# Kernel tuning notes

Hardware: AMD Instinct MI355X
Metric: run time of the kernel (lower is better)

## Reference

```python
import jax, jax.numpy as jnp
import numpy as np

H, D = 8, 16
NA, NB, E, F = 50000, 50000, 200000, 128
SQRT_D = float(np.sqrt(D))


def _proj(x, W, b):
    # Linear then split heads: [N, F] -> [N, H, D]
    return (x @ W + b).reshape(x.shape[0], H, D)


def _seg_softmax(alpha, idx, n):
    # softmax over edges sharing the same destination node (per head)
    amax = jax.ops.segment_max(alpha, idx, num_segments=n)
    amax = jnp.where(jnp.isfinite(amax), amax, 0.0)
    ex = jnp.exp(alpha - amax[idx])
    den = jax.ops.segment_sum(ex, idx, num_segments=n)
    return ex / (den[idx] + 1e-16)


def _hgt_conv(xa, xb, eis, Wk, bk, Wq, bq, Wv, bv, Wa, ba, skip, arel, mrel, prel):
    # node types: 0='a', 1='b'; edge types: 0 a->b, 1 b->a, 2 a->a
    xs = (xa, xb)
    k = [_proj(xs[t], Wk[t], bk[t]) for t in range(2)]
    q = [_proj(xs[t], Wq[t], bq[t]) for t in range(2)]
    v = [_proj(xs[t], Wv[t], bv[t]) for t in range(2)]
    nn_ = (xa.shape[0], xb.shape[0])
    agg = [jnp.zeros((nn_[t], H, D), xa.dtype) for t in range(2)]
    spec = ((0, 1, eis[0]), (1, 0, eis[1]), (0, 0, eis[2]))
    for e, (s, d, ei) in enumerate(spec):
        src, dst = ei[0], ei[1]
        k_rel = jnp.einsum('nhd,hde->nhe', k[s], arel[e])  # [Ns,H,D]
        v_rel = jnp.einsum('nhd,hde->nhe', v[s], mrel[e])
        alpha = jnp.sum(q[d][dst] * k_rel[src], axis=-1) * prel[e] / SQRT_D  # [E,H]
        w = _seg_softmax(alpha, dst, nn_[d])
        agg[d] = agg[d] + jax.ops.segment_sum(v_rel[src] * w[..., None], dst, num_segments=nn_[d])
    outs = []
    for t in range(2):
        o = jax.nn.gelu(agg[t].reshape(-1, H * D), approximate=False) @ Wa[t] + ba[t]
        sgate = jax.nn.sigmoid(skip[t])  # learned skip-gate, dims match so always applied
        outs.append(sgate * o + (1.0 - sgate) * xs[t])
    return outs[0], outs[1]


def _forward(xa, xb, eis, Wk, bk, Wq, bq, Wv, bv, Wa, ba, skip, arel, mrel, prel):
    for l in range(2):
        xa, xb = _hgt_conv(xa, xb, eis, Wk[l], bk[l], Wq[l], bq[l], Wv[l], bv[l],
                           Wa[l], ba[l], skip[l], arel[l], mrel[l], prel[l])
        if l < 1:
            xa, xb = jax.nn.relu(xa), jax.nn.relu(xb)  # dropout: identity in eval mode
    return xa, xb


def setup_inputs() -> dict:
    key = jax.random.key(0)
    ks = jax.random.split(key, 12)
    s = 0.05
    return {
        'xa': jax.random.normal(ks[0], (NA, F), jnp.float32),
        'xb': jax.random.normal(ks[1], (NB, F), jnp.float32),
        'ei_ab': jax.random.randint(ks[2], (2, E), 0, NA, dtype=jnp.int32),
        'ei_ba': jax.random.randint(ks[3], (2, E), 0, NB, dtype=jnp.int32),
        'ei_aa': jax.random.randint(ks[4], (2, E), 0, NA, dtype=jnp.int32),
        'Wk': jax.random.normal(ks[5], (2, 2, F, F), jnp.float32) * s,
        'bk': jnp.zeros((2, 2, F), jnp.float32),
        'Wq': jax.random.normal(ks[6], (2, 2, F, F), jnp.float32) * s,
        'bq': jnp.zeros((2, 2, F), jnp.float32),
        'Wv': jax.random.normal(ks[7], (2, 2, F, F), jnp.float32) * s,
        'bv': jnp.zeros((2, 2, F), jnp.float32),
        'Wa': jax.random.normal(ks[8], (2, 2, F, F), jnp.float32) * s,
        'ba': jnp.zeros((2, 2, F), jnp.float32),
        'skip': jnp.zeros((2, 2), jnp.float32),
        'arel': jax.random.normal(ks[9], (2, 3, H, D, D), jnp.float32) * (1.0 / SQRT_D),
        'mrel': jax.random.normal(ks[10], (2, 3, H, D, D), jnp.float32) * (1.0 / SQRT_D),
        'prel': jnp.ones((2, 3, H), jnp.float32),
    }


def reference(xa, xb, ei_ab, ei_ba, ei_aa, Wk, bk, Wq, bq, Wv, bv, Wa, ba, skip, arel, mrel, prel):
    return _forward(xa, xb, (ei_ab, ei_ba, ei_aa), Wk, bk, Wq, bq, Wv, bv, Wa, ba, skip, arel, mrel, prel)
```

## Files before the change

### kernel.cpp

```cpp
#include <hip/hip_runtime.h>
#include <hip/hip_bf16.h>
#include <math.h>

#define F 128
#define NH 8
#define HD 16

static inline int cdiv(int a, int b) { return (a + b - 1) / b; }

typedef __attribute__((ext_vector_type(8))) short bf16x8;
typedef __attribute__((ext_vector_type(4))) float f32x4;

__device__ __forceinline__ float geluf(float x) {
    return 0.5f * x * (1.f + erff(x * 0.70710678118654752440f));
}

__device__ __forceinline__ short f2bf(float f) {
    __hip_bfloat16 h = __float2bfloat16(f);
    return *reinterpret_cast<short*>(&h);
}

__device__ __forceinline__ float bflo(unsigned int u) { return __uint_as_float(u << 16); }
__device__ __forceinline__ float bfhi(unsigned int u) { return __uint_as_float(u & 0xffff0000u); }
__device__ __forceinline__ float bf2f(short s) {
    return __uint_as_float(((unsigned int)(unsigned short)s) << 16);
}
__device__ __forceinline__ unsigned int packbf(float a, float b) {
    return (unsigned int)(unsigned short)f2bf(a) | ((unsigned int)(unsigned short)f2bf(b) << 16);
}

__device__ __forceinline__ void glds16(const void* g, void* l) {
    __builtin_amdgcn_global_load_lds(
        (const __attribute__((address_space(1))) unsigned int*)g,
        (__attribute__((address_space(3))) unsigned int*)l, 16, 0, 0);
}

__device__ __forceinline__ void slot_info(int slot, int& kind, int& wsel, int& e, int& t) {
    switch (slot) {
        case 0: kind = 0; wsel = 0; t = 0; e = 0; break;
        case 1: kind = 1; wsel = 1; t = 0; e = 0; break;
        case 2: kind = 1; wsel = 2; t = 0; e = 0; break;
        case 3: kind = 1; wsel = 1; t = 0; e = 2; break;
        case 4: kind = 1; wsel = 2; t = 0; e = 2; break;
        case 5: kind = 0; wsel = 0; t = 1; e = 0; break;
        case 6: kind = 1; wsel = 1; t = 1; e = 1; break;
        case 7: kind = 1; wsel = 2; t = 1; e = 1; break;
        case 8: kind = 0; wsel = 3; t = 0; e = 0; break;
        default: kind = 0; wsel = 3; t = 1; e = 0; break;
    }
}

__global__ void prep_all(const float* __restrict__ Wk, const float* __restrict__ bk,
                         const float* __restrict__ Wq, const float* __restrict__ bq,
                         const float* __restrict__ Wv, const float* __restrict__ bv,
                         const float* __restrict__ Wa, const float* __restrict__ ba,
                         const float* __restrict__ arel, const float* __restrict__ mrel,
                         const float* __restrict__ xa, const float* __restrict__ xb,
                         const int* __restrict__ ei0, const int* __restrict__ ei1,
                         const int* __restrict__ ei2,
                         short* __restrict__ Wslots, float* __restrict__ bslots,
                         short* __restrict__ xab, short* __restrict__ xbb,
                         int* __restrict__ cnt,
                         int NA_, int NB_, int E0, int E1, int E2,
                         int PWB, int CONVB) {
    const int WTOT = 10 * 16384;
    const int bid = blockIdx.x;
    const int tid = threadIdx.x;
    if (bid < 2 * PWB) {
        const int layer = bid / PWB;
        short* Wl = Wslots + (size_t)layer * WTOT;
        float* bl = bslots + (size_t)layer * 10 * 128;
        int idx = (bid % PWB) * 256 + tid;
        if (idx < WTOT) {
            int slot = idx >> 14, rem = idx & 16383;
            int n = rem >> 7, k = rem & 127;
            int kind, wsel, e, t;
            slot_info(slot, kind, wsel, e, t);
            float out;
            if (kind == 0) {
                const float* Wb = (wsel == 0 ? Wq : Wa) + (size_t)(layer * 2 + t) * 16384;
                out = Wb[k * 128 + n];
            } else {
                int h = n >> 4, j = n & 15;
                const float* Wb = (wsel == 1 ? Wk : Wv) + (size_t)(layer * 2 + t) * 16384;
                const float* R = (wsel == 1 ? arel : mrel) + (size_t)((layer * 3 + e) * NH + h) * 256;
                float s = 0.f;
                #pragma unroll
                for (int d = 0; d < HD; ++d) s += Wb[k * 128 + h * 16 + d] * R[d * 16 + j];
                out = s;
            }
            int chunk = k >> 3, kin = k & 7;
            int cph = (chunk + (n & 15)) & 15;
            Wl[(size_t)slot * 16384 + n * 128 + cph * 8 + kin] = f2bf(out);
        } else {
            int r = idx - WTOT;
            if (r < 10 * 128) {
                int slot = r >> 7, n = r & 127;
                int kind, wsel, e, t;
                slot_info(slot, kind, wsel, e, t);
                float out;
                if (kind == 0) {
                    const float* bb = (wsel == 0 ? bq : ba) + (size_t)(layer * 2 + t) * 128;
                    out = bb[n];
                } else {
                    int h = n >> 4, j = n & 15;
                    const float* bb = (wsel == 1 ? bk : bv) + (size_t)(layer * 2 + t) * 128;
                    const float* R = (wsel == 1 ? arel : mrel) + (size_t)((layer * 3 + e) * NH + h) * 256;
                    float s = 0.f;
                    #pragma unroll
                    for (int d = 0; d < HD; ++d) s += bb[h * 16 + d] * R[d * 16 + j];
                    out = s;
                }
                bl[slot * 128 + n] = out;
            }
        }
    } else if (bid < 2 * PWB + CONVB) {
        int gi = (bid - 2 * PWB) * 256 + tid;
        int total8 = (NA_ + NB_) * 16;
        if (gi < total8) {
            size_t e = (size_t)gi * 8;
            const float* src; short* dst; size_t off;
            if (e < (size_t)NA_ * 128) { src = xa; dst = xab; off = e; }
            else { src = xb; dst = xbb; off = e - (size_t)NA_ * 128; }
            float4 v0 = *(const float4*)&src[off];
            float4 v1 = *(const float4*)&src[off + 4];
            bf16x8 s;
            s[0] = f2bf(v0.x); s[1] = f2bf(v0.y); s[2] = f2bf(v0.z); s[3] = f2bf(v0.w);
            s[4] = f2bf(v1.x); s[5] = f2bf(v1.y); s[6] = f2bf(v1.z); s[7] = f2bf(v1.w);
            *(bf16x8*)&dst[off] = s;
        }
    } else {
        int i = (bid - 2 * PWB - CONVB) * 256 + tid;
        if (i >= E0 + E1 + E2) return;
        const int* ei; int li, Ee, base;
        if (i < E0)           { li = i;           ei = ei0; Ee = E0; base = 0; }
        else if (i < E0 + E1) { li = i - E0;      ei = ei1; Ee = E1; base = NB_; }
        else                  { li = i - E0 - E1; ei = ei2; Ee = E2; base = NB_ + NA_; }
        atomicAdd(&cnt[base + ei[Ee + li]], 1);
    }
}

__device__ __forceinline__ short* qkv_slot_ptr(int side, int s,
    short* qA, short* kA0, short* vA0, short* kA2, short* vA2,
    short* qB, short* kB1, short* vB1) {
    if (side) {
        if (s == 0) return qB;
        if (s == 1) return kB1;
        return vB1;
    }
    if (s == 0) return qA;
    if (s == 1) return kA0;
    if (s == 2) return vA0;
    if (s == 3) return kA2;
    return vA2;
}

__device__ __forceinline__ void stage_W(const short* __restrict__ Wt, short* Ws,
                                        int wave, int lane) {
    #pragma unroll
    for (int it = 0; it < 8; ++it) {
        int off = (it * 4 + wave) * 1024;
        glds16((const char*)Wt + off + lane * 16, (char*)Ws + off);
    }
}

__global__ __launch_bounds__(256) void gemm_qkv_all(
    const short* __restrict__ Aa, const short* __restrict__ Ab,
    const short* __restrict__ Wl, const float* __restrict__ bl,
    short* __restrict__ qA, short* __restrict__ kA0, short* __restrict__ vA0,
    short* __restrict__ kA2, short* __restrict__ vA2,
    short* __restrict__ qB, short* __restrict__ kB1, short* __restrict__ vB1,
    int NA_, int NB_, int nbA, int nbGemm,
    const int* __restrict__ cnt, int* __restrict__ offc, int* __restrict__ bsum, int NT) {
    __shared__ __align__(16) float Wsf[64 * 132];
    __shared__ __align__(16) short As[64 * 136];
    __shared__ int slds[256];
    short* Ws = (short*)Wsf;
    const int tid = threadIdx.x;
    const int bid = blockIdx.x;

    if (bid >= nbGemm) {
        int blk = bid - nbGemm;
        int i = blk * 256 + tid;
        int v = (i < NT) ? cnt[i] : 0;
        slds[tid] = v;
        __syncthreads();
        #pragma unroll
        for (int s = 1; s < 256; s <<= 1) {
            int t = (tid >= s) ? slds[tid - s] : 0;
            __syncthreads();
            slds[tid] += t;
            __syncthreads();
        }
        if (i < NT) offc[i] = slds[tid] - v;
        if (tid == 255) bsum[blk] = slds[255];
        return;
    }

    const int side = bid >= nbA;
    const short* A = side ? Ab : Aa;
    const int N = side ? NB_ : NA_;
    const int row0 = (side ? bid - nbA : bid) * 64;
    const short* Wbase = Wl + (side ? (size_t)5 * 16384 : 0);
    const float* bbase = bl + (side ? 5 * 128 : 0);
    const int S = side ? 3 : 5;

    const int wave = tid >> 6;
    const int lane = tid & 63;
    const int m16 = lane & 15;
    const int kg = lane >> 4;
    const int arow = wave * 16 + m16;

    #pragma unroll
    for (int it = 0; it < 4; ++it) {
        int chunk = tid + it * 256;
        int r = chunk >> 4, c8 = (chunk & 15) * 8;
        int gr = row0 + r;
        bf16x8 s = {};
        if (gr < N) s = *(const bf16x8*)&A[(size_t)gr * F + c8];
        *(bf16x8*)&As[r * 136 + c8] = s;
    }
    __syncthreads();

    bf16x8 af[4];
    #pragma unroll
    for (int kq = 0; kq < 4; ++kq)
        af[kq] = *(const bf16x8*)&As[arow * 136 + kq * 32 + kg * 8];

    for (int s = 0; s < S; ++s) {
        if (s) __syncthreads();
        stage_W(Wbase + (size_t)s * 16384, Ws, wave, lane);
        __syncthreads();

        f32x4 acc[8] = {};
        #pragma unroll
        for (int kq = 0; kq < 4; ++kq) {
            #pragma unroll
            for (int nt = 0; nt < 8; ++nt) {
                int cph = (kq * 4 + kg + m16) & 15;
                bf16x8 b = *(const bf16x8*)&Ws[(nt * 16 + m16) * 128 + cph * 8];
                acc[nt] = __builtin_amdgcn_mfma_f32_16x16x32_bf16(af[kq], b, acc[nt], 0, 0, 0);
            }
        }
        __syncthreads();

        #pragma unroll
        for (int nt = 0; nt < 8; ++nt)
            #pragma unroll
            for (int r = 0; r < 4; ++r)
                Wsf[(wave * 16 + kg * 4 + r) * 132 + nt * 16 + m16] = acc[nt][r];
        __syncthreads();

        short* optr = qkv_slot_ptr(side, s, qA, kA0, vA0, kA2, vA2, qB, kB1, vB1);
        const float* bias = bbase + s * 128;
        #pragma unroll
        for (int it = 0; it < 4; ++it) {
            int chunk = tid + it * 256;
            int r = chunk >> 4, c8 = (chunk & 15) * 8;
            int gr = row0 + r;
            if (gr >= N) continue;
            float4 b0 = *(const float4*)&bias[c8];
            float4 b1 = *(const float4*)&bias[c8 + 4];
            float4 va = *(float4*)&Wsf[r * 132 + c8];
            float4 vb = *(float4*)&Wsf[r * 132 + c8 + 4];
            bf16x8 o;
            o[0] = f2bf(va.x + b0.x); o[1] = f2bf(va.y + b0.y);
            o[2] = f2bf(va.z + b0.z); o[3] = f2bf(va.w + b0.w);
            o[4] = f2bf(vb.x + b1.x); o[5] = f2bf(vb.y + b1.y);
            o[6] = f2bf(vb.z + b1.z); o[7] = f2bf(vb.w + b1.w);
            *(bf16x8*)&optr[(size_t)gr * F + c8] = o;
        }
    }
}

__global__ __launch_bounds__(256) void fused_out_qkv(
    const short* __restrict__ aggA, const short* __restrict__ aggB,
    const short* __restrict__ Wl0, const float* __restrict__ bl0,
    const short* __restrict__ xabA, const short* __restrict__ xabB,
    const float* __restrict__ skipp,
    const short* __restrict__ Wl1, const float* __restrict__ bl1,
    short* __restrict__ x1A, short* __restrict__ x1B,
    short* __restrict__ qA, short* __restrict__ kA0, short* __restrict__ vA0,
    short* __restrict__ kA2, short* __restrict__ vA2,
    short* __restrict__ qB, short* __restrict__ kB1, short* __restrict__ vB1,
    int NA_, int NB_, int nbA) {
    __shared__ __align__(16) float Wsf[64 * 132];
    __shared__ __align__(16) short As[64 * 136];
    short* Ws = (short*)Wsf;
    const int tid = threadIdx.x;
    const int bid = blockIdx.x;
    const int side = bid >= nbA;
    const short* A = side ? aggB : aggA;
    const int N = side ? NB_ : NA_;
    const int row0 = (side ? bid - nbA : bid) * 64;
    const short* Wt0 = Wl0 + (size_t)(side ? 9 : 8) * 16384;
    const float* bias0 = bl0 + (side ? 9 : 8) * 128;

    const int wave = tid >> 6;
    const int lane = tid & 63;
    const int m16 = lane & 15;
    const int kg = lane >> 4;
    const int arow = wave * 16 + m16;

    stage_W(Wt0, Ws, wave, lane);
    #pragma unroll
    for (int it = 0; it < 4; ++it) {
        int chunk = tid + it * 256;
        int r = chunk >> 4, c8 = (chunk & 15) * 8;
        int gr = row0 + r;
        bf16x8 s = {};
        if (gr < N) {
            s = *(const bf16x8*)&A[(size_t)gr * F + c8];
            #pragma unroll
            for (int u = 0; u < 8; ++u) s[u] = f2bf(geluf(bf2f(s[u])));
        }
        *(bf16x8*)&As[r * 136 + c8] = s;
    }
    __syncthreads();

    {
        f32x4 acc[8] = {};
        #pragma unroll
        for (int kq = 0; kq < 4; ++kq) {
            bf16x8 a = *(const bf16x8*)&As[arow * 136 + kq * 32 + kg * 8];
            #pragma unroll
            for (int nt = 0; nt < 8; ++nt) {
                int cph = (kq * 4 + kg + m16) & 15;
                bf16x8 b = *(const bf16x8*)&Ws[(nt * 16 + m16) * 128 + cph * 8];
                acc[nt] = __builtin_amdgcn_mfma_f32_16x16x32_bf16(a, b, acc[nt], 0, 0, 0);
            }
        }
        __syncthreads();
        #pragma unroll
        for (int nt = 0; nt < 8; ++nt)
            #pragma unroll
            for (int r = 0; r < 4; ++r)
                Wsf[(wave * 16 + kg * 4 + r) * 132 + nt * 16 + m16] = acc[nt][r];
        __syncthreads();
    }

    {
        float sg = 1.f / (1.f + expf(-skipp[side]));
        short* x1 = side ? x1B : x1A;
        const short* xf = side ? xabB : xabA;
        #pragma unroll
        for (int it = 0; it < 4; ++it) {
            int chunk = tid + it * 256;
            int r = chunk >> 4, c8 = (chunk & 15) * 8;
            int gr = row0 + r;
            if (gr >= N) continue;
            float4 b0 = *(const float4*)&bias0[c8];
            float4 b1 = *(const float4*)&bias0[c8 + 4];
            float4 va = *(float4*)&Wsf[r * 132 + c8];
            float4 vb = *(float4*)&Wsf[r * 132 + c8 + 4];
            bf16x8 xrv = *(const bf16x8*)&xf[(size_t)gr * F + c8];
            float v[8] = {va.x + b0.x, va.y + b0.y, va.z + b0.z, va.w + b0.w,
                          vb.x + b1.x, vb.y + b1.y, vb.z + b1.z, vb.w + b1.w};
            bf16x8 o;
            #pragma unroll
            for (int u = 0; u < 8; ++u)
                o[u] = f2bf(fmaxf(sg * v[u] + (1.f - sg) * bf2f(xrv[u]), 0.f));
            *(bf16x8*)&x1[(size_t)gr * F + c8] = o;
            *(bf16x8*)&As[r * 136 + c8] = o;
        }
    }
    __syncthreads();

    bf16x8 af[4];
    #pragma unroll
    for (int kq = 0; kq < 4; ++kq)
        af[kq] = *(const bf16x8*)&As[arow * 136 + kq * 32 + kg * 8];

    const short* Wbase = Wl1 + (side ? (size_t)5 * 16384 : 0);
    const float* bbase = bl1 + (side ? 5 * 128 : 0);
    const int S = side ? 3 : 5;

    for (int s = 0; s < S; ++s) {
        __syncthreads();
        stage_W(Wbase + (size_t)s * 16384, Ws, wave, lane);
        __syncthreads();

        f32x4 acc[8] = {};
        #pragma unroll
        for (int kq = 0; kq < 4; ++kq) {
            #pragma unroll
            for (int nt = 0; nt < 8; ++nt) {
                int cph = (kq * 4 + kg + m16) & 15;
                bf16x8 b = *(const bf16x8*)&Ws[(nt * 16 + m16) * 128 + cph * 8];
                acc[nt] = __builtin_amdgcn_mfma_f32_16x16x32_bf16(af[kq], b, acc[nt], 0, 0, 0);
            }
        }
        __syncthreads();

        #pragma unroll
        for (int nt = 0; nt < 8; ++nt)
            #pragma unroll
            for (int r = 0; r < 4; ++r)
                Wsf[(wave * 16 + kg * 4 + r) * 132 + nt * 16 + m16] = acc[nt][r];
        __syncthreads();

        short* optr = qkv_slot_ptr(side, s, qA, kA0, vA0, kA2, vA2, qB, kB1, vB1);
        const float* bias = bbase + s * 128;
        #pragma unroll
        for (int it = 0; it < 4; ++it) {
            int chunk = tid + it * 256;
            int r = chunk >> 4, c8 = (chunk & 15) * 8;
            int gr = row0 + r;
            if (gr >= N) continue;
            float4 b0 = *(const float4*)&bias[c8];
            float4 b1 = *(const float4*)&bias[c8 + 4];
            float4 va = *(float4*)&Wsf[r * 132 + c8];
            float4 vb = *(float4*)&Wsf[r * 132 + c8 + 4];
            bf16x8 o;
            o[0] = f2bf(va.x + b0.x); o[1] = f2bf(va.y + b0.y);
            o[2] = f2bf(va.z + b0.z); o[3] = f2bf(va.w + b0.w);
            o[4] = f2bf(vb.x + b1.x); o[5] = f2bf(vb.y + b1.y);
            o[6] = f2bf(vb.z + b1.z); o[7] = f2bf(vb.w + b1.w);
            *(bf16x8*)&optr[(size_t)gr * F + c8] = o;
        }
    }
}

__global__ __launch_bounds__(256) void gemm_out_final(
    const short* __restrict__ aggA, const short* __restrict__ aggB,
    const short* __restrict__ Wl, const float* __restrict__ bl,
    const short* __restrict__ xbA, const short* __restrict__ xbB,
    const float* __restrict__ skipp,
    float* __restrict__ CfA, float* __restrict__ CfB,
    int NA_, int NB_, int nbA) {
    __shared__ __align__(16) float Wsf[64 * 132];
    __shared__ __align__(16) short As[64 * 136];
    short* Ws = (short*)Wsf;
    const int tid = threadIdx.x;
    const int bid = blockIdx.x;
    const int side = bid >= nbA;
    const short* A = side ? aggB : aggA;
    const int N = side ? NB_ : NA_;
    const int row0 = (side ? bid - nbA : bid) * 64;
    const short* Wt = Wl + (size_t)(side ? 9 : 8) * 16384;
    const float* bias = bl + (side ? 9 : 8) * 128;

    const int wave = tid >> 6;
    const int lane = tid & 63;
    const int m16 = lane & 15;
    const int kg = lane >> 4;
    const int arow = wave * 16 + m16;

    stage_W(Wt, Ws, wave, lane);
    #pragma unroll
    for (int it = 0; it < 4; ++it) {
        int chunk = tid + it * 256;
        int r = chunk >> 4, c8 = (chunk & 15) * 8;
        int gr = row0 + r;
        bf16x8 s = {};
        if (gr < N) {
            s = *(const bf16x8*)&A[(size_t)gr * F + c8];
            #pragma unroll
            for (int u = 0; u < 8; ++u) s[u] = f2bf(geluf(bf2f(s[u])));
        }
        *(bf16x8*)&As[r * 136 + c8] = s;
    }
    __syncthreads();

    f32x4 acc[8] = {};
    #pragma unroll
    for (int kq = 0; kq < 4; ++kq) {
        bf16x8 a = *(const bf16x8*)&As[arow * 136 + kq * 32 + kg * 8];
        #pragma unroll
        for (int nt = 0; nt < 8; ++nt) {
            int cph = (kq * 4 + kg + m16) & 15;
            bf16x8 b = *(const bf16x8*)&Ws[(nt * 16 + m16) * 128 + cph * 8];
            acc[nt] = __builtin_amdgcn_mfma_f32_16x16x32_bf16(a, b, acc[nt], 0, 0, 0);
        }
    }
    __syncthreads();

    #pragma unroll
    for (int nt = 0; nt < 8; ++nt)
        #pragma unroll
        for (int r = 0; r < 4; ++r)
            Wsf[(wave * 16 + kg * 4 + r) * 132 + nt * 16 + m16] = acc[nt][r];
    __syncthreads();

    float sg = 1.f / (1.f + expf(-skipp[side]));
    #pragma unroll
    for (int it = 0; it < 4; ++it) {
        int chunk = tid + it * 256;
        int r = chunk >> 4, c8 = (chunk & 15) * 8;
        int gr = row0 + r;
        if (gr >= N) continue;
        float4 b0 = *(const float4*)&bias[c8];
        float4 b1 = *(const float4*)&bias[c8 + 4];
        float4 va = *(float4*)&Wsf[r * 132 + c8];
        float4 vb = *(float4*)&Wsf[r * 132 + c8 + 4];
        float v[8] = {va.x + b0.x, va.y + b0.y, va.z + b0.z, va.w + b0.w,
                      vb.x + b1.x, vb.y + b1.y, vb.z + b1.z, vb.w + b1.w};
        const short* xb = side ? xbB : xbA;
        bf16x8 xrv = *(const bf16x8*)&xb[(size_t)gr * F + c8];
        float* Cf = side ? CfB : CfA;
        float o[8];
        #pragma unroll
        for (int u = 0; u < 8; ++u)
            o[u] = sg * v[u] + (1.f - sg) * bf2f(xrv[u]);
        *(float4*)&Cf[(size_t)gr * F + c8]     = make_float4(o[0], o[1], o[2], o[3]);
        *(float4*)&Cf[(size_t)gr * F + c8 + 4] = make_float4(o[4], o[5], o[6], o[7]);
    }
}


__global__ __launch_bounds__(1024) void scan2(int* __restrict__ bsum, int nb,
                                              int* __restrict__ off_n) {
    __shared__ int lds[1024];
    int tid = threadIdx.x;
    int v = (tid < nb) ? bsum[tid] : 0;
    lds[tid] = v;
    __syncthreads();
    #pragma unroll
    for (int s = 1; s < 1024; s <<= 1) {
        int t = (tid >= s) ? lds[tid - s] : 0;
        __syncthreads();
        lds[tid] += t;
        __syncthreads();
    }
    if (tid < nb) bsum[tid] = lds[tid] - v;
    if (tid == 1023) *off_n = lds[1023];
}

__global__ void scan3(int* __restrict__ off, int* __restrict__ woff,
                      const int* __restrict__ bsum, int n) {
    int i = blockIdx.x * 256 + threadIdx.x;
    if (i < n) {
        int v = off[i] + bsum[blockIdx.x];
        off[i] = v;
        woff[i] = v;
    }
}

__global__ void scatter_all(const int* __restrict__ ei0, const int* __restrict__ ei1,
                            const int* __restrict__ ei2, int E0, int E1, int E2,
                            int NB_, int NA_, int* __restrict__ woff,
                            int* __restrict__ csr_src) {
    int i = blockIdx.x * 256 + threadIdx.x;
    if (i >= E0 + E1 + E2) return;
    const int* ei; int li, Ee, base;
    if (i < E0)           { li = i;           ei = ei0; Ee = E0; base = 0; }
    else if (i < E0 + E1) { li = i - E0;      ei = ei1; Ee = E1; base = NB_; }
    else                  { li = i - E0 - E1; ei = ei2; Ee = E2; base = NB_ + NA_; }
    int p = atomicAdd(&woff[base + ei[Ee + li]], 1);
    csr_src[p] = ei[li] * 16;
}

__device__ __forceinline__ void seg_set4(
    const uint4* __restrict__ kArr, const uint4* __restrict__ vArr,
    int c0, int e1, const int* __restrict__ csr, int s, int p,
    const float* __restrict__ qf, float pr,
    float* __restrict__ accv, float& den) {
    for (; c0 < e1; c0 += 4) {
        int rem = e1 - c0;
        bool act = s < rem;
        int sj = csr[c0 + (act ? s : 0)];
        uint4 kw = kArr[sj + p];
        uint4 vw = vArr[sj + p];
        float d = bflo(kw.x) * qf[0];
        d = fmaf(bfhi(kw.x), qf[1], d);
        d = fmaf(bflo(kw.y), qf[2], d);
        d = fmaf(bfhi(kw.y), qf[3], d);
        d = fmaf(bflo(kw.z), qf[4], d);
        d = fmaf(bfhi(kw.z), qf[5], d);
        d = fmaf(bflo(kw.w), qf[6], d);
        d = fmaf(bfhi(kw.w), qf[7], d);
        d += __shfl_xor(d, 1);
        float ex = __expf(fminf(d * pr, 80.f));
        ex = act ? ex : 0.f;
        den += ex;
        accv[0] = fmaf(ex, bflo(vw.x), accv[0]);
        accv[1] = fmaf(ex, bfhi(vw.x), accv[1]);
        accv[2] = fmaf(ex, bflo(vw.y), accv[2]);
        accv[3] = fmaf(ex, bfhi(vw.y), accv[3]);
        accv[4] = fmaf(ex, bflo(vw.z), accv[4]);
        accv[5] = fmaf(ex, bfhi(vw.z), accv[5]);
        accv[6] = fmaf(ex, bflo(vw.w), accv[6]);
        accv[7] = fmaf(ex, bfhi(vw.w), accv[7]);
    }
}

__device__ __forceinline__ void seg_fold(float* __restrict__ accv, float& den,
                                         float* __restrict__ r) {
    #pragma unroll
    for (int j = 0; j < 8; ++j) {
        accv[j] += __shfl_xor(accv[j], 16);
        accv[j] += __shfl_xor(accv[j], 32);
    }
    den += __shfl_xor(den, 16);
    den += __shfl_xor(den, 32);
    float inv = 1.f / (den + 1e-16f);
    #pragma unroll
    for (int j = 0; j < 8; ++j) r[j] = fmaf(accv[j], inv, r[j]);
}

__global__ __launch_bounds__(256) void seg_attn_all(
    const short* __restrict__ qA, const short* __restrict__ kA0,
    const short* __restrict__ vA0, const short* __restrict__ kA2,
    const short* __restrict__ vA2, const short* __restrict__ qB,
    const short* __restrict__ kB1, const short* __restrict__ vB1,
    const int* __restrict__ off0, const int* __restrict__ off1,
    const int* __restrict__ off2, const int* __restrict__ csrS,
    const float* __restrict__ prelL,
    short* __restrict__ aggA, short* __restrict__ aggB,
    int NA_, int NB_, int nba) {
    const int wv = threadIdx.x >> 6;
    const int l = threadIdx.x & 63;
    const int s = l >> 4;
    const int p = l & 15;
    const int h = p >> 1;
    const int isA = (int)blockIdx.x < nba;
    int dst = (isA ? blockIdx.x : blockIdx.x - nba) * 4 + wv;
    if (dst >= (isA ? NA_ : NB_)) return;

    uint4 qw = ((const uint4*)(isA ? qA : qB))[(size_t)dst * 16 + p];
    float qf[8] = {bflo(qw.x), bfhi(qw.x), bflo(qw.y), bfhi(qw.y),
                   bflo(qw.z), bfhi(qw.z), bflo(qw.w), bfhi(qw.w)};

    float r[8] = {};
    float accv[8] = {};
    float den = 0.f;
    if (isA) {
        seg_set4((const uint4*)kB1, (const uint4*)vB1, off1[dst], off1[dst + 1],
                 csrS, s, p, qf, prelL[1 * NH + h] * 0.25f, accv, den);
        seg_fold(accv, den, r);
        #pragma unroll
        for (int j = 0; j < 8; ++j) accv[j] = 0.f;
        den = 0.f;
        seg_set4((const uint4*)kA2, (const uint4*)vA2, off2[dst], off2[dst + 1],
                 csrS, s, p, qf, prelL[2 * NH + h] * 0.25f, accv, den);
        seg_fold(accv, den, r);
    } else {
        seg_set4((const uint4*)kA0, (const uint4*)vA0, off0[dst], off0[dst + 1],
                 csrS, s, p, qf, prelL[0 * NH + h] * 0.25f, accv, den);
        seg_fold(accv, den, r);
    }
    if (s == 0) {
        uint4 o;
        o.x = packbf(r[0], r[1]);
        o.y = packbf(r[2], r[3]);
        o.z = packbf(r[4], r[5]);
        o.w = packbf(r[6], r[7]);
        ((uint4*)(isA ? aggA : aggB))[(size_t)dst * 16 + p] = o;
    }
}

extern "C" void kernel_launch(void* const* d_in, const int* in_sizes, int n_in,
                              void* d_out, int out_size, void* d_ws, size_t ws_size,
                              hipStream_t stream) {
    const float* xa   = (const float*)d_in[0];
    const float* xb   = (const float*)d_in[1];
    const int* ei_ab  = (const int*)d_in[2];
    const int* ei_ba  = (const int*)d_in[3];
    const int* ei_aa  = (const int*)d_in[4];
    const float* Wk   = (const float*)d_in[5];
    const float* bk   = (const float*)d_in[6];
    const float* Wq   = (const float*)d_in[7];
    const float* bq   = (const float*)d_in[8];
    const float* Wv   = (const float*)d_in[9];
    const float* bv   = (const float*)d_in[10];
    const float* Wa   = (const float*)d_in[11];
    const float* ba   = (const float*)d_in[12];
    const float* skip = (const float*)d_in[13];
    const float* arel = (const float*)d_in[14];
    const float* mrel = (const float*)d_in[15];
    const float* prel = (const float*)d_in[16];

    const int NA = in_sizes[0] / F;
    const int NB = in_sizes[1] / F;
    const int E0 = in_sizes[2] / 2, E1 = in_sizes[3] / 2, E2 = in_sizes[4] / 2;
    const int ET = E0 + E1 + E2;
    const int NT = NB + NA + NA;

    float* ws = (float*)d_ws;
    size_t o = 0;
    float* bslots = ws + o; o += 2 * 10 * 128;
    int* iws = (int*)(ws + o);
    size_t io = 0;
    int* cnt   = iws + io; io += NT;
    int* bsum  = iws + io; io += 1024;
    int* offc  = iws + io; io += NT + 1;
    int* woff  = iws + io; io += NT;
    int* csrS  = iws + io; io += ET;
    io = (io + 7) & ~(size_t)7;
    short* sws = (short*)(iws + io);
    size_t so = 0;
    short* qA  = sws + so; so += (size_t)NA * 128;
    short* kA0 = sws + so; so += (size_t)NA * 128;
    short* vA0 = sws + so; so += (size_t)NA * 128;
    short* kA2 = sws + so; so += (size_t)NA * 128;
    short* vA2 = sws + so; so += (size_t)NA * 128;
    short* qB  = sws + so; so += (size_t)NB * 128;
    short* kB1 = sws + so; so += (size_t)NB * 128;
    short* vB1 = sws + so; so += (size_t)NB * 128;
    short* aggA = sws + so; so += (size_t)NA * 128;
    short* aggB = sws + so; so += (size_t)NB * 128;
    short* x1ab = sws + so; so += (size_t)NA * 128;
    short* x1bb = sws + so; so += (size_t)NB * 128;
    short* xab  = sws + so; so += (size_t)NA * 128;
    short* xbb  = sws + so; so += (size_t)NB * 128;
    short* Wslots = sws + so; so += (size_t)2 * 10 * 16384;

    float* outA = (float*)d_out;
    float* outB = (float*)d_out + (size_t)NA * F;

    const int PWB = cdiv(10 * 16384 + 10 * 128, 256);
    const int CONVB = cdiv((NA + NB) * 16, 256);
    const int HISTB = cdiv(ET, 256);
    const int nbA64 = cdiv(NA, 64), nbB64 = cdiv(NB, 64);
    const int nbGemm = nbA64 + nbB64;
    const int nbScan = cdiv(NT, 256);
    const int nba4 = cdiv(NA, 4), nbb4 = cdiv(NB, 4);

    const short* Wl0 = Wslots;
    const short* Wl1 = Wslots + (size_t)10 * 16384;
    const float* bl0 = bslots;
    const float* bl1 = bslots + 10 * 128;

    hipMemsetAsync(cnt, 0, (size_t)NT * sizeof(int), stream);

    prep_all<<<2 * PWB + CONVB + HISTB, 256, 0, stream>>>(
        Wk, bk, Wq, bq, Wv, bv, Wa, ba, arel, mrel, xa, xb,
        ei_ab, ei_ba, ei_aa, Wslots, bslots, xab, xbb, cnt,
        NA, NB, E0, E1, E2, PWB, CONVB);

    gemm_qkv_all<<<nbGemm + nbScan, 256, 0, stream>>>(
        xab, xbb, Wl0, bl0, qA, kA0, vA0, kA2, vA2, qB, kB1, vB1,
        NA, NB, nbA64, nbGemm, cnt, offc, bsum, NT);

    scan2<<<1, 1024, 0, stream>>>(bsum, nbScan, offc + NT);
    scan3<<<nbScan, 256, 0, stream>>>(offc, woff, bsum, NT);
    scatter_all<<<HISTB, 256, 0, stream>>>(ei_ab, ei_ba, ei_aa, E0, E1, E2, NB, NA, woff, csrS);

    const int* off_e0 = offc;
    const int* off_e1 = offc + NB;
    const int* off_e2 = offc + NB + NA;

    seg_attn_all<<<nba4 + nbb4, 256, 0, stream>>>(
        qA, kA0, vA0, kA2, vA2, qB, kB1, vB1,
        off_e0, off_e1, off_e2, csrS, prel, aggA, aggB, NA, NB, nba4);

    fused_out_qkv<<<nbA64 + nbB64, 256, 0, stream>>>(
        aggA, aggB, Wl0, bl0, xab, xbb, skip, Wl1, bl1,
        x1ab, x1bb, qA, kA0, vA0, kA2, vA2, qB, kB1, vB1, NA, NB, nbA64);

    seg_attn_all<<<nba4 + nbb4, 256, 0, stream>>>(
        qA, kA0, vA0, kA2, vA2, qB, kB1, vB1,
        off_e0, off_e1, off_e2, csrS, prel + 3 * NH, aggA, aggB, NA, NB, nba4);

    gemm_out_final<<<nbA64 + nbB64, 256, 0, stream>>>(
        aggA, aggB, Wl1, bl1, x1ab, x1bb, skip + 2, outA, outB, NA, NB, nbA64);
}
```

Before: 340.0 us.

## Prefetch next weight slice into registers while computing the current GEMM slice

The per-slice weight staging through global-to-LDS copies is replaced by a register prefetch of the next 128x128 weight slice, issued before the MFMA loop of the current slice and written to LDS after the epilogue. The goal is to hide the global load latency of weight staging behind MFMA and epilogue work in both the QKV GEMM and the fused output+QKV kernels. In exchange it costs 32 extra VGPRs per thread for the prefetch buffer, which may reduce occupancy. The first slice is now staged before the A-tile load.

```diff
diff --git a/kernel.cpp b/kernel.cpp
--- a/kernel.cpp
+++ b/kernel.cpp
@@ -164,6 +164,18 @@
     }
 }
 
+__device__ __forceinline__ void prefetch_W(const short* __restrict__ Wt,
+                                           uint4* wreg, int wave, int lane) {
+    #pragma unroll
+    for (int it = 0; it < 8; ++it)
+        wreg[it] = *(const uint4*)((const char*)Wt + (it * 4 + wave) * 1024 + lane * 16);
+}
+__device__ __forceinline__ void write_W(short* Ws, const uint4* wreg, int wave, int lane) {
+    #pragma unroll
+    for (int it = 0; it < 8; ++it)
+        *(uint4*)((char*)Ws + (it * 4 + wave) * 1024 + lane * 16) = wreg[it];
+}
+
 __global__ __launch_bounds__(256) void gemm_qkv_all(
     const short* __restrict__ Aa, const short* __restrict__ Ab,
     const short* __restrict__ Wl, const float* __restrict__ bl,
@@ -211,6 +223,7 @@
     const int kg = lane >> 4;
     const int arow = wave * 16 + m16;
 
+    stage_W(Wbase, Ws, wave, lane);
     #pragma unroll
     for (int it = 0; it < 4; ++it) {
         int chunk = tid + it * 256;
@@ -227,10 +240,10 @@
     for (int kq = 0; kq < 4; ++kq)
         af[kq] = *(const bf16x8*)&As[arow * 136 + kq * 32 + kg * 8];
 
+    uint4 wreg[8];
     for (int s = 0; s < S; ++s) {
-        if (s) __syncthreads();
-        stage_W(Wbase + (size_t)s * 16384, Ws, wave, lane);
-        __syncthreads();
+        if (s + 1 < S)
+            prefetch_W(Wbase + (size_t)(s + 1) * 16384, wreg, wave, lane);
 
         f32x4 acc[8] = {};
         #pragma unroll
@@ -269,6 +282,11 @@
             o[4] = f2bf(vb.x + b1.x); o[5] = f2bf(vb.y + b1.y);
             o[6] = f2bf(vb.z + b1.z); o[7] = f2bf(vb.w + b1.w);
             *(bf16x8*)&optr[(size_t)gr * F + c8] = o;
+        }
+        if (s + 1 < S) {
+            __syncthreads();
+            write_W(Ws, wreg, wave, lane);
+            __syncthreads();
         }
     }
 }
@@ -302,6 +320,10 @@
     const int kg = lane >> 4;
     const int arow = wave * 16 + m16;
 
+    const short* Wbase = Wl1 + (side ? (size_t)5 * 16384 : 0);
+    const float* bbase = bl1 + (side ? 5 * 128 : 0);
+    const int S = side ? 3 : 5;
+
     stage_W(Wt0, Ws, wave, lane);
     #pragma unroll
     for (int it = 0; it < 4; ++it) {
@@ -317,6 +339,9 @@
         *(bf16x8*)&As[r * 136 + c8] = s;
     }
     __syncthreads();
+
+    uint4 wreg[8];
+    prefetch_W(Wbase, wreg, wave, lane);
 
     {
         f32x4 acc[8] = {};
@@ -366,19 +391,17 @@
     }
     __syncthreads();
 
+    write_W(Ws, wreg, wave, lane);
+    __syncthreads();
+
     bf16x8 af[4];
     #pragma unroll
     for (int kq = 0; kq < 4; ++kq)
         af[kq] = *(const bf16x8*)&As[arow * 136 + kq * 32 + kg * 8];
 
-    const short* Wbase = Wl1 + (side ? (size_t)5 * 16384 : 0);
-    const float* bbase = bl1 + (side ? 5 * 128 : 0);
-    const int S = side ? 3 : 5;
-
     for (int s = 0; s < S; ++s) {
-        __syncthreads();
-        stage_W(Wbase + (size_t)s * 16384, Ws, wave, lane);
-        __syncthreads();
+        if (s + 1 < S)
+            prefetch_W(Wbase + (size_t)(s + 1) * 16384, wreg, wave, lane);
 
         f32x4 acc[8] = {};
         #pragma unroll
@@ -417,6 +440,11 @@
             o[4] = f2bf(vb.x + b1.x); o[5] = f2bf(vb.y + b1.y);
             o[6] = f2bf(vb.z + b1.z); o[7] = f2bf(vb.w + b1.w);
             *(bf16x8*)&optr[(size_t)gr * F + c8] = o;
+        }
+        if (s + 1 < S) {
+            __syncthreads();
+            write_W(Ws, wreg, wave, lane);
+            __syncthreads();
         }
     }
 }
```

Measured after the change: 414.5 us. 21.9% more time.
